# Kernel optimization log

Hardware: AMD Instinct MI355X
Metric: run time of the kernel (lower is better)

## Reference

```python
import jax, jax.numpy as jnp
import numpy as np

N, C, T, V = 16, 256, 256, 64   # batch, node_channel_in, time, total_nodes
SC, SV = 3, 64                  # node_channel_out, num_seeds
NEW_NODES, C_OUT = 64, 3
IN_DIM = C * V + SC * SV        # 16576


def setup_inputs() -> dict:
    key = jax.random.key(0)
    k1, k2, k3, k4 = jax.random.split(key, 4)
    x = jax.random.normal(k1, (N, C, T, V), dtype=jnp.float32)
    seeds = jax.random.normal(k2, (N, T, SC, SV), dtype=jnp.float32)
    # Stacked weights of the `new_nodes` independent Linear(IN_DIM, C_OUT) layers
    W = jax.random.normal(k3, (NEW_NODES, C_OUT, IN_DIM), dtype=jnp.float32) * 0.02
    b = jax.random.normal(k4, (NEW_NODES, C_OUT), dtype=jnp.float32) * 0.02
    return {"x": x, "seeds": seeds, "W": W, "b": b}


def reference(x, seeds, W, b):
    n, c, t, v = x.shape
    # (n,c,t,v) -> (n,t,c*v)
    xm = jnp.transpose(x, (0, 2, 1, 3)).reshape(n, t, c * v)
    sm = seeds.reshape(n, t, -1)                 # (n,t,sc*sv)
    mix = jnp.concatenate([xm, sm], axis=2)      # (n,t,IN_DIM)
    # Fused horizontal GEMM over all new_nodes projections, then stacked on dim 3:
    # out[n,t,c_out,j] = sum_k mix[n,t,k] * W[j,c_out,k] + b[j,c_out]
    out = jnp.einsum('ntk,jck->ntcj', mix, W) + b.T[None, None]
    return out  # (n, t, node_channel_out, new_nodes)
```

## Files before the change

kernel.cpp:

```cpp
#include <hip/hip_runtime.h>
#include <hip/hip_bf16.h>

typedef unsigned short u16;
typedef unsigned int   u32;
typedef __attribute__((ext_vector_type(8))) short bf16x8;
typedef __attribute__((ext_vector_type(4))) float f32x4;

#define NB    16
#define CIN   256
#define TDIM  256
#define VDIM  64
#define PCOL  192
#define NCHX  256
#define NCH   259
#define MTOT  4096
#define CHUNK_U16 12288
#define WT_BYTES ((size_t)NCH * CHUNK_U16 * 2)

__device__ __forceinline__ u16 f2bf(float f) {
  u32 u = __builtin_bit_cast(u32, f);
  u32 r = u + 0x7fffu + ((u >> 16) & 1u);
  return (u16)(r >> 16);
}
__device__ __forceinline__ u32 pk2(float a, float b) {
  return (u32)f2bf(a) | ((u32)f2bf(b) << 16);
}
__device__ __forceinline__ void gload_lds16(const void* g, void* l) {
  __builtin_amdgcn_global_load_lds(
      (const __attribute__((address_space(1))) u32*)g,
      (__attribute__((address_space(3))) u32*)l, 16, 0, 0);
}

__global__ void prep_w(const float* __restrict__ W, u16* __restrict__ Wt) {
  int u  = blockIdx.x * 256 + threadIdx.x;
  int q  = u & 7;
  int p  = (u >> 3) % PCOL;
  int ch = u / (PCOL * 8);
  int j = p & 63, co = p >> 6;
  const float* src = W + (size_t)(j * 3 + co) * 16576 + ch * 64 + q * 8;
  float4 fa = *(const float4*)src;
  float4 fb = *(const float4*)(src + 4);
  uint4 v;
  v.x = pk2(fa.x, fa.y); v.y = pk2(fa.z, fa.w);
  v.z = pk2(fb.x, fb.y); v.w = pk2(fb.z, fb.w);
  ((uint4*)Wt)[(size_t)ch * 1536 + p * 8 + (q ^ (p & 7))] = v;
}

__global__ __launch_bounds__(256, 2)
void gemm_bf16(const float* __restrict__ x, const float* __restrict__ seeds,
               const u16* __restrict__ Wt, float* __restrict__ dst,
               const float* __restrict__ bias, int S) {
  __shared__ __align__(16) u16 lds[2][16384];
  const int tid  = threadIdx.x;
  const int lane = tid & 63;
  const int wid  = tid >> 6;
  const int bid  = blockIdx.x;
  int mblk, ksp;
  if (S == 8) { ksp = bid & 7;  mblk = bid >> 3; }
  else        { mblk = bid & 63; ksp = bid >> 6; }
  const int n  = mblk >> 2;
  const int t0 = (mblk & 3) << 6;
  const int c0 = (NCH * ksp) / S;
  const int c1 = (NCH * (ksp + 1)) / S;

  const int q0 = tid & 7;
  const int m0 = tid >> 3;

  f32x4 acc[4][3] = {};

  auto STAGE = [&](int buf, int ch) {
    const char* gsrc = (const char*)Wt + (size_t)ch * 24576 + wid * 1024 + lane * 16;
    char* lbase = (char*)&lds[buf][4096] + wid * 1024;
    #pragma unroll
    for (int r = 0; r < 6; ++r)
      gload_lds16(gsrc + (size_t)r * 4096, lbase + r * 4096);
    #pragma unroll
    for (int r = 0; r < 2; ++r) {
      int m = m0 + 32 * r;
      const float* arow;
      if (ch < NCHX)
        arow = x + (((size_t)n * CIN + ch) * TDIM + (t0 + m)) * VDIM + q0 * 8;
      else
        arow = seeds + ((size_t)n * TDIM + (t0 + m)) * 192 + (ch - NCHX) * 64 + q0 * 8;
      float4 fa = *(const float4*)arow;
      float4 fb = *(const float4*)(arow + 4);
      uint4 v;
      v.x = pk2(fa.x, fa.y); v.y = pk2(fa.z, fa.w);
      v.z = pk2(fb.x, fb.y); v.w = pk2(fb.z, fb.w);
      ((uint4*)&lds[buf][0])[m * 8 + (q0 ^ (m & 7))] = v;
    }
  };

  const int lr = lane & 15, lq = lane >> 4;

  auto COMPUTE = [&](int buf) {
    const u16* L = &lds[buf][0];
    #pragma unroll
    for (int ks = 0; ks < 2; ++ks) {
      const int q = ks * 4 + lq;
      bf16x8 af[4], bfr[3];
      #pragma unroll
      for (int mt = 0; mt < 4; ++mt) {
        int m = mt * 16 + lr;
        af[mt] = *(const bf16x8*)(L + (m * 8 + (q ^ (m & 7))) * 8);
      }
      #pragma unroll
      for (int nt = 0; nt < 3; ++nt) {
        int p = wid * 48 + nt * 16 + lr;
        bfr[nt] = *(const bf16x8*)(L + 4096 + (p * 8 + (q ^ (p & 7))) * 8);
      }
      #pragma unroll
      for (int mt = 0; mt < 4; ++mt)
        #pragma unroll
        for (int nt = 0; nt < 3; ++nt)
          acc[mt][nt] = __builtin_amdgcn_mfma_f32_16x16x32_bf16(
              af[mt], bfr[nt], acc[mt][nt], 0, 0, 0);
    }
  };

  int buf = 0;
  STAGE(0, c0);
  for (int ch = c0; ch < c1; ++ch) {
    __syncthreads();
    if (ch + 1 < c1) STAGE(buf ^ 1, ch + 1);
    COMPUTE(buf);
    buf ^= 1;
  }

  float* dbase = dst + (size_t)ksp * MTOT * PCOL;
  #pragma unroll
  for (int mt = 0; mt < 4; ++mt)
    #pragma unroll
    for (int nt = 0; nt < 3; ++nt) {
      int col = wid * 48 + nt * 16 + lr;
      float bv = bias ? bias[(col & 63) * 3 + (col >> 6)] : 0.f;
      #pragma unroll
      for (int r = 0; r < 4; ++r) {
        int row = mblk * 64 + mt * 16 + lq * 4 + r;
        dbase[(size_t)row * PCOL + col] = acc[mt][nt][r] + bv;
      }
    }
}

__global__ void reduce_k(const float* __restrict__ part, const float* __restrict__ b,
                         float* __restrict__ out, int S) {
  int i4 = (blockIdx.x * 256 + threadIdx.x) * 4;
  float4 a = *(const float4*)&part[i4];
  for (int s = 1; s < S; ++s) {
    const float4 v = *(const float4*)&part[(size_t)s * (MTOT * PCOL) + i4];
    a.x += v.x; a.y += v.y; a.z += v.z; a.w += v.w;
  }
  int p0 = i4 % PCOL;
  a.x += b[((p0 + 0) & 63) * 3 + ((p0 + 0) >> 6)];
  a.y += b[((p0 + 1) & 63) * 3 + ((p0 + 1) >> 6)];
  a.z += b[((p0 + 2) & 63) * 3 + ((p0 + 2) >> 6)];
  a.w += b[((p0 + 3) & 63) * 3 + ((p0 + 3) >> 6)];
  *(float4*)&out[i4] = a;
}

__global__ void fallback_k(const float* __restrict__ x, const float* __restrict__ seeds,
                           const float* __restrict__ W, const float* __restrict__ b,
                           float* __restrict__ out) {
  __shared__ float mk[512];
  int m = blockIdx.x, n = m >> 8, t = m & 255, p = threadIdx.x;
  float acc = 0.f;
  for (int k0 = 0; k0 < 16576; k0 += 512) {
    int kn = min(512, 16576 - k0);
    __syncthreads();
    for (int i = threadIdx.x; i < kn; i += 256) {
      int k = k0 + i;
      mk[i] = (k < 16384)
                ? x[(((size_t)n * 256 + (k >> 6)) * 256 + t) * 64 + (k & 63)]
                : seeds[((size_t)n * 256 + t) * 192 + (k - 16384)];
    }
    __syncthreads();
    if (p < PCOL) {
      const float* wr = W + (size_t)((p & 63) * 3 + (p >> 6)) * 16576 + k0;
      for (int i = 0; i < kn; ++i) acc += mk[i] * wr[i];
    }
  }
  if (p < PCOL) out[(size_t)m * PCOL + p] = acc + b[(p & 63) * 3 + (p >> 6)];
}

extern "C" void kernel_launch(void* const* d_in, const int* in_sizes, int n_in,
                              void* d_out, int out_size, void* d_ws, size_t ws_size,
                              hipStream_t stream) {
  (void)in_sizes; (void)n_in; (void)out_size;
  const float* x     = (const float*)d_in[0];
  const float* seeds = (const float*)d_in[1];
  const float* W     = (const float*)d_in[2];
  const float* b     = (const float*)d_in[3];
  float* out = (float*)d_out;

  if (ws_size < WT_BYTES) {
    fallback_k<<<dim3(MTOT), dim3(256), 0, stream>>>(x, seeds, W, b, out);
    return;
  }
  u16* Wt = (u16*)d_ws;
  int S = 8;
  while (S > 1 && WT_BYTES + (size_t)S * MTOT * PCOL * 4 > ws_size) S >>= 1;
  if (WT_BYTES + (size_t)S * MTOT * PCOL * 4 > ws_size) S = 1;

  prep_w<<<dim3((NCH * PCOL * 8) / 256), dim3(256), 0, stream>>>(W, Wt);
  if (S == 1) {
    gemm_bf16<<<dim3(64), dim3(256), 0, stream>>>(x, seeds, Wt, out, b, 1);
  } else {
    float* part = (float*)((char*)d_ws + WT_BYTES);
    gemm_bf16<<<dim3(64 * S), dim3(256), 0, stream>>>(x, seeds, Wt, part, nullptr, S);
    reduce_k<<<dim3(MTOT * PCOL / 4 / 256), dim3(256), 0, stream>>>(part, b, out, S);
  }
}
```

Before: 95.26 us.

## Prefetch A tiles into registers two chunks ahead with explicit waitcnt pipeline

Splits staging into separate B (global-to-LDS) and A (global-to-register) loads, so the fp32 activation loads for chunk ch+2 are issued before the MFMA compute of chunk ch. Conversion to bf16 and the LDS write happen after compute. Hand-placed vmcnt/lgkmcnt waits and sched_barriers replace __syncthreads, keeping loads in flight across compute. This hides global load latency for A, which the old loop exposed, but raises register pressure and relies on exact waitcnt counting being correct.

```diff
diff --git a/kernel.cpp b/kernel.cpp
--- a/kernel.cpp
+++ b/kernel.cpp
@@ -68,31 +68,40 @@
 
   f32x4 acc[4][3] = {};
 
-  auto STAGE = [&](int buf, int ch) {
+  struct ASet { float4 r0a, r0b, r1a, r1b; };
+  ASet AX, AY;
+
+  auto Bi = [&](int ch, int buf) {
     const char* gsrc = (const char*)Wt + (size_t)ch * 24576 + wid * 1024 + lane * 16;
     char* lbase = (char*)&lds[buf][4096] + wid * 1024;
     #pragma unroll
     for (int r = 0; r < 6; ++r)
       gload_lds16(gsrc + (size_t)r * 4096, lbase + r * 4096);
-    #pragma unroll
-    for (int r = 0; r < 2; ++r) {
-      int m = m0 + 32 * r;
-      const float* arow;
-      if (ch < NCHX)
-        arow = x + (((size_t)n * CIN + ch) * TDIM + (t0 + m)) * VDIM + q0 * 8;
-      else
-        arow = seeds + ((size_t)n * TDIM + (t0 + m)) * 192 + (ch - NCHX) * 64 + q0 * 8;
-      float4 fa = *(const float4*)arow;
-      float4 fb = *(const float4*)(arow + 4);
-      uint4 v;
-      v.x = pk2(fa.x, fa.y); v.y = pk2(fa.z, fa.w);
-      v.z = pk2(fb.x, fb.y); v.w = pk2(fb.z, fb.w);
-      ((uint4*)&lds[buf][0])[m * 8 + (q0 ^ (m & 7))] = v;
-    }
+  };
+  auto Ai = [&](int ch, ASet& s) {
+    const float *a0, *a1;
+    if (ch < NCHX) {
+      a0 = x + (((size_t)n * CIN + ch) * TDIM + (t0 + m0)) * VDIM + q0 * 8;
+      a1 = a0 + (size_t)32 * VDIM;
+    } else {
+      a0 = seeds + ((size_t)n * TDIM + (t0 + m0)) * 192 + (ch - NCHX) * 64 + q0 * 8;
+      a1 = a0 + (size_t)32 * 192;
+    }
+    s.r0a = *(const float4*)a0; s.r0b = *(const float4*)(a0 + 4);
+    s.r1a = *(const float4*)a1; s.r1b = *(const float4*)(a1 + 4);
+  };
+  auto CONV = [&](const ASet& s, int buf) {
+    uint4 v;
+    v.x = pk2(s.r0a.x, s.r0a.y); v.y = pk2(s.r0a.z, s.r0a.w);
+    v.z = pk2(s.r0b.x, s.r0b.y); v.w = pk2(s.r0b.z, s.r0b.w);
+    ((uint4*)&lds[buf][0])[m0 * 8 + (q0 ^ (m0 & 7))] = v;
+    int m1 = m0 + 32;
+    v.x = pk2(s.r1a.x, s.r1a.y); v.y = pk2(s.r1a.z, s.r1a.w);
+    v.z = pk2(s.r1b.x, s.r1b.y); v.w = pk2(s.r1b.z, s.r1b.w);
+    ((uint4*)&lds[buf][0])[m1 * 8 + (q0 ^ (m1 & 7))] = v;
   };
 
   const int lr = lane & 15, lq = lane >> 4;
-
   auto COMPUTE = [&](int buf) {
     const u16* L = &lds[buf][0];
     #pragma unroll
@@ -118,14 +127,44 @@
     }
   };
 
-  int buf = 0;
-  STAGE(0, c0);
-  for (int ch = c0; ch < c1; ++ch) {
-    __syncthreads();
-    if (ch + 1 < c1) STAGE(buf ^ 1, ch + 1);
-    COMPUTE(buf);
-    buf ^= 1;
-  }
+  Bi(c0, 0);
+  __builtin_amdgcn_sched_barrier(0);
+  Ai(c0, AX);
+  if (c0 + 1 < c1) Ai(c0 + 1, AY);
+  __builtin_amdgcn_sched_barrier(0);
+  CONV(AX, 0);
+  asm volatile("s_waitcnt lgkmcnt(0)" ::: "memory");
+  __builtin_amdgcn_sched_barrier(0);
+  __builtin_amdgcn_s_barrier();
+  __builtin_amdgcn_sched_barrier(0);
+
+#define PHASE(BUF, AP, AN)                                                    \
+  {                                                                           \
+    const bool hasN  = (ch + 1 < c1);                                         \
+    const bool hasNN = (ch + 2 < c1);                                         \
+    if (hasN)  Bi(ch + 1, (BUF) ^ 1);                                         \
+    __builtin_amdgcn_sched_barrier(0);                                        \
+    if (hasNN) Ai(ch + 2, AN);                                                \
+    __builtin_amdgcn_sched_barrier(0);                                        \
+    COMPUTE(BUF);                                                             \
+    if (!hasN) break;                                                         \
+    CONV(AP, (BUF) ^ 1);                                                      \
+    if (hasNN) { asm volatile("s_waitcnt vmcnt(4)" ::: "memory"); }           \
+    else       { asm volatile("s_waitcnt vmcnt(0)" ::: "memory"); }           \
+    asm volatile("s_waitcnt lgkmcnt(0)" ::: "memory");                        \
+    __builtin_amdgcn_sched_barrier(0);                                        \
+    __builtin_amdgcn_s_barrier();                                             \
+    __builtin_amdgcn_sched_barrier(0);                                        \
+  }
+
+  int ch = c0;
+  while (true) {
+    PHASE(0, AY, AX)
+    ++ch;
+    PHASE(1, AX, AY)
+    ++ch;
+  }
+#undef PHASE
 
   float* dbase = dst + (size_t)ksp * MTOT * PCOL;
   #pragma unroll
```

New measurement: 81.40 us. -14.6%, faster.
